# Kernel tuning notes

Hardware: AMD Instinct MI355X
Metric: run time of the kernel (lower is better)

## Reference

```python
import jax, jax.numpy as jnp
import numpy as np

C = 64
B, H, W = 2, 96, 96
EPS = 1e-5  # BatchNorm2d default eps


def conv1x1(x, w, b):
    # x: [B,C,H,W], w: [O,C], b: [O] -> [B,O,H,W]
    return jnp.einsum('bchw,oc->bohw', x, w) + b[None, :, None, None]


def setup_inputs() -> dict:
    key = jax.random.key(0)
    ks = jax.random.split(key, 12)
    s = 1.0 / np.sqrt(C)
    return {
        'x': jax.random.normal(ks[0], (B, C, H, W), dtype=jnp.float32),
        'g_w': jax.random.normal(ks[1], (C, C), dtype=jnp.float32) * s,
        'g_b': jax.random.normal(ks[2], (C,), dtype=jnp.float32) * s,
        'theta_w': jax.random.normal(ks[3], (C, C), dtype=jnp.float32) * s,
        'theta_b': jax.random.normal(ks[4], (C,), dtype=jnp.float32) * s,
        'phi_w': jax.random.normal(ks[5], (C, C), dtype=jnp.float32) * s,
        'phi_b': jax.random.normal(ks[6], (C,), dtype=jnp.float32) * s,
        'w_w': jax.random.normal(ks[7], (C, C), dtype=jnp.float32) * s,
        'w_b': jax.random.normal(ks[8], (C,), dtype=jnp.float32) * s,
        'bn_gamma': jnp.ones((C,), dtype=jnp.float32),
        'bn_beta': jnp.zeros((C,), dtype=jnp.float32),
        'bn_mean': jax.random.normal(ks[9], (C,), dtype=jnp.float32) * 0.1,
        'bn_var': jax.random.uniform(ks[10], (C,), dtype=jnp.float32, minval=0.5, maxval=1.5),
    }


def reference(x, g_w, g_b, theta_w, theta_b, phi_w, phi_b, w_w, w_b,
              bn_gamma, bn_beta, bn_mean, bn_var):
    b, c, h, w = x.shape
    n = h * w
    # 1x1 conv Q/K/V projections, flattened over spatial
    g_x = conv1x1(x, g_w, g_b).reshape(b, c, n).transpose(0, 2, 1)        # [B,N,C]
    theta_x = conv1x1(x, theta_w, theta_b).reshape(b, c, n).transpose(0, 2, 1)  # [B,N,C]
    phi_x = conv1x1(x, phi_w, phi_b).reshape(b, c, n)                      # [B,C,N]
    # full NxN attention: f = theta @ phi, softmax over last dim, y = f @ g
    f = jnp.einsum('bnc,bcm->bnm', theta_x, phi_x)                         # [B,N,N]
    attn = jax.nn.softmax(f, axis=-1)
    y = jnp.einsum('bnm,bmc->bnc', attn, g_x)                              # [B,N,C]
    y = y.transpose(0, 2, 1).reshape(b, c, h, w)
    # W: 1x1 conv + BatchNorm2d (inference: running stats) + residual
    w_y = conv1x1(y, w_w, w_b)
    inv_std = jax.lax.rsqrt(bn_var + EPS)
    w_y = (w_y - bn_mean[None, :, None, None]) * (bn_gamma * inv_std)[None, :, None, None] \
          + bn_beta[None, :, None, None]
    return w_y + x
```

## Files before the change

### kernel.cpp

```cpp
#include <hip/hip_runtime.h>
#include <hip/hip_bf16.h>

#define CC 64
#define NN 9216
#define NB 2
#define NQT 288
#define NKT 144

typedef __attribute__((ext_vector_type(4))) float f32x4;
typedef __attribute__((ext_vector_type(8))) short bf16x8;
typedef __attribute__((ext_vector_type(4))) unsigned int u32x4;

static __device__ __forceinline__ short f2bf(float f) {
    union { float f; unsigned u; } a; a.f = f;
    unsigned r = a.u + 0x7FFFu + ((a.u >> 16) & 1u);
    return (short)(r >> 16);
}

__global__ __launch_bounds__(256) void proj_kernel(
    const float* __restrict__ x,
    const float* __restrict__ gw, const float* __restrict__ gb,
    const float* __restrict__ tw, const float* __restrict__ tb,
    const float* __restrict__ pw, const float* __restrict__ pb,
    short* __restrict__ Qw, short* __restrict__ Kw, short* __restrict__ Vw)
{
    __shared__ float xs[64][68];
    const int b  = blockIdx.x / (NN / 64);
    const int n0 = (blockIdx.x % (NN / 64)) * 64;
    const int t  = threadIdx.x;

    {
        const int c = t >> 2, q = t & 3;
        const float* src = x + ((size_t)b * CC + c) * NN + n0 + q * 16;
        #pragma unroll
        for (int i = 0; i < 4; ++i) {
            float4 v = ((const float4*)src)[i];
            xs[c][q * 16 + i * 4 + 0] = v.x;
            xs[c][q * 16 + i * 4 + 1] = v.y;
            xs[c][q * 16 + i * 4 + 2] = v.z;
            xs[c][q * 16 + i * 4 + 3] = v.w;
        }
    }
    __syncthreads();

    const int n  = t & 63;
    const int og = __builtin_amdgcn_readfirstlane(t >> 6);
    float xr[64];
    #pragma unroll
    for (int c = 0; c < 64; ++c) xr[c] = xs[c][n];

    bf16x8 qv0, qv1, kv0, kv1;
    #pragma unroll
    for (int oi = 0; oi < 16; ++oi) {
        const int o = og * 16 + oi;
        float a0 = gb[o], a1 = tb[o], a2 = pb[o];
        #pragma unroll
        for (int c = 0; c < 64; ++c) {
            const float xv = xr[c];
            a0 += gw[o * 64 + c] * xv;
            a1 += tw[o * 64 + c] * xv;
            a2 += pw[o * 64 + c] * xv;
        }
        Vw[((size_t)b * CC + o) * NN + n0 + n] = f2bf(a0);
        if (oi < 8) { qv0[oi] = f2bf(a1); kv0[oi] = f2bf(a2); }
        else        { qv1[oi - 8] = f2bf(a1); kv1[oi - 8] = f2bf(a2); }
    }
    const size_t qkbase = ((size_t)b * NN + n0 + n) * CC + og * 16;
    *(bf16x8*)&Qw[qkbase]     = qv0;
    *(bf16x8*)&Qw[qkbase + 8] = qv1;
    *(bf16x8*)&Kw[qkbase]     = kv0;
    *(bf16x8*)&Kw[qkbase + 8] = kv1;
}

template<int SP>
__global__ __launch_bounds__(256) void attn_kernel(
    const short* __restrict__ Qw, const short* __restrict__ Kw,
    const short* __restrict__ Vw, float* __restrict__ Yp,
    float* __restrict__ Mp, float* __restrict__ Sp)
{
    constexpr int KCH = NKT / SP;
    const int gw  = blockIdx.x * 4 + (threadIdx.x >> 6);
    const int l   = threadIdx.x & 63;
    const int lr  = l & 15, lg = l >> 4;
    const int qt  = gw % NQT;
    const int rem = gw / NQT;
    const int b   = rem & 1;
    const int s   = rem >> 1;
    const int q0  = qt * 32;

    const short* Qb = Qw + (size_t)b * NN * CC;
    const short* Kb = Kw + (size_t)b * NN * CC;
    const short* Vb = Vw + (size_t)b * CC * NN;

    bf16x8 qf[2][2];
    #pragma unroll
    for (int qg = 0; qg < 2; ++qg)
        #pragma unroll
        for (int ch = 0; ch < 2; ++ch)
            qf[qg][ch] = *(const bf16x8*)(Qb + (size_t)(q0 + qg * 16 + lr) * CC + ch * 32 + lg * 8);

    f32x4 yacc[2][4];
    #pragma unroll
    for (int qg = 0; qg < 2; ++qg)
        #pragma unroll
        for (int u = 0; u < 4; ++u) yacc[qg][u] = (f32x4){0.f, 0.f, 0.f, 0.f};
    float m[2]  = {-1e30f, -1e30f};
    float se[2] = {0.f, 0.f};

    for (int kt = s * KCH; kt < s * KCH + KCH; ++kt) {
        const int jb = kt * 64;
        bf16x8 kf[4][2], vf[4][2];
        #pragma unroll
        for (int tt = 0; tt < 4; ++tt)
            #pragma unroll
            for (int ch = 0; ch < 2; ++ch)
                kf[tt][ch] = *(const bf16x8*)(Kb + (size_t)(jb + tt * 16 + lr) * CC + ch * 32 + lg * 8);
        #pragma unroll
        for (int u = 0; u < 4; ++u)
            #pragma unroll
            for (int jg = 0; jg < 2; ++jg)
                vf[u][jg] = *(const bf16x8*)(Vb + (size_t)(u * 16 + lr) * NN + jb + jg * 32 + lg * 8);

        #pragma unroll
        for (int qg = 0; qg < 2; ++qg) {
            f32x4 sv[4];
            #pragma unroll
            for (int tt = 0; tt < 4; ++tt) {
                f32x4 a = (f32x4){0.f, 0.f, 0.f, 0.f};
                a = __builtin_amdgcn_mfma_f32_16x16x32_bf16(kf[tt][0], qf[qg][0], a, 0, 0, 0);
                a = __builtin_amdgcn_mfma_f32_16x16x32_bf16(kf[tt][1], qf[qg][1], a, 0, 0, 0);
                sv[tt] = a;
            }
            float mx = -1e30f;
            #pragma unroll
            for (int tt = 0; tt < 4; ++tt)
                #pragma unroll
                for (int r = 0; r < 4; ++r) mx = fmaxf(mx, sv[tt][r]);
            mx = fmaxf(mx, __shfl_xor(mx, 16));
            mx = fmaxf(mx, __shfl_xor(mx, 32));
            const float mnew = fmaxf(m[qg], mx);
            const float scal = __expf(m[qg] - mnew);
            float rs = 0.f;
            unsigned p2[4][2];
            #pragma unroll
            for (int tt = 0; tt < 4; ++tt) {
                const float pa = __expf(sv[tt][0] - mnew);
                const float pb2 = __expf(sv[tt][1] - mnew);
                const float pc = __expf(sv[tt][2] - mnew);
                const float pd = __expf(sv[tt][3] - mnew);
                rs += (pa + pb2) + (pc + pd);
                p2[tt][0] = (unsigned)(unsigned short)f2bf(pa) | ((unsigned)(unsigned short)f2bf(pb2) << 16);
                p2[tt][1] = (unsigned)(unsigned short)f2bf(pc) | ((unsigned)(unsigned short)f2bf(pd) << 16);
            }
            rs += __shfl_xor(rs, 16);
            rs += __shfl_xor(rs, 32);
            se[qg] = se[qg] * scal + rs;
            m[qg]  = mnew;
            #pragma unroll
            for (int u = 0; u < 4; ++u) yacc[qg][u] *= scal;

            #pragma unroll
            for (int jg = 0; jg < 2; ++jg) {
                unsigned bfr[4];
                #pragma unroll
                for (int q = 0; q < 4; ++q) {
                    const int qh = q >> 1, h = q & 1;
                    const int src = lr | ((((lg << 1) + qh) & 3) << 4);
                    const int c0 = __shfl((int)p2[jg * 2 + 0][h], src);
                    const int c1 = __shfl((int)p2[jg * 2 + 1][h], src);
                    bfr[q] = (unsigned)((lg & 2) ? c1 : c0);
                }
                u32x4 bt = {bfr[0], bfr[1], bfr[2], bfr[3]};
                const bf16x8 pbf = __builtin_bit_cast(bf16x8, bt);
                #pragma unroll
                for (int u = 0; u < 4; ++u)
                    yacc[qg][u] = __builtin_amdgcn_mfma_f32_16x16x32_bf16(vf[u][jg], pbf, yacc[qg][u], 0, 0, 0);
            }
        }
    }

    const size_t pbase = (size_t)(s * NB + b) * NN;
    #pragma unroll
    for (int qg = 0; qg < 2; ++qg) {
        const int n = q0 + qg * 16 + lr;
        float* yrow = Yp + (pbase + n) * CC;
        #pragma unroll
        for (int u = 0; u < 4; ++u)
            *(f32x4*)&yrow[u * 16 + lg * 4] = yacc[qg][u];
        if (lg == 0) { Mp[pbase + n] = m[qg]; Sp[pbase + n] = se[qg]; }
    }
}

template<int SP>
__global__ __launch_bounds__(256) void out_kernel(
    const float* __restrict__ Yp, const float* __restrict__ Mp,
    const float* __restrict__ Sp, const float* __restrict__ x,
    const float* __restrict__ ww, const float* __restrict__ wb,
    const float* __restrict__ gam, const float* __restrict__ bet,
    const float* __restrict__ mu, const float* __restrict__ var,
    float* __restrict__ out)
{
    __shared__ float ys[64][65];
    __shared__ float wgt[SP][64];
    __shared__ float scl[64], shf[64];
    const int b  = blockIdx.x / (NN / 64);
    const int n0 = (blockIdx.x % (NN / 64)) * 64;
    const int t  = threadIdx.x;

    if (t < 64) {
        float e[SP], ssv[SP];
        float M = -1e30f;
        #pragma unroll
        for (int s = 0; s < SP; ++s) {
            e[s]   = Mp[(size_t)(s * NB + b) * NN + n0 + t];
            ssv[s] = Sp[(size_t)(s * NB + b) * NN + n0 + t];
            M = fmaxf(M, e[s]);
        }
        float den = 0.f;
        #pragma unroll
        for (int s = 0; s < SP; ++s) { e[s] = __expf(e[s] - M); den += e[s] * ssv[s]; }
        const float inv = 1.f / den;
        #pragma unroll
        for (int s = 0; s < SP; ++s) wgt[s][t] = e[s] * inv;
    } else if (t < 128) {
        const int c = t - 64;
        const float sc = gam[c] * rsqrtf(var[c] + 1e-5f);
        scl[c] = sc;
        shf[c] = bet[c] + (wb[c] - mu[c]) * sc;
    }
    __syncthreads();

    {
        const int n = t >> 2, q = t & 3;
        float acc[16];
        #pragma unroll
        for (int i = 0; i < 16; ++i) acc[i] = 0.f;
        #pragma unroll
        for (int s = 0; s < SP; ++s) {
            const float w = wgt[s][n];
            const float* src = Yp + ((size_t)(s * NB + b) * NN + n0 + n) * CC + q * 16;
            #pragma unroll
            for (int i = 0; i < 4; ++i) {
                const float4 v = ((const float4*)src)[i];
                acc[i * 4 + 0] += w * v.x;
                acc[i * 4 + 1] += w * v.y;
                acc[i * 4 + 2] += w * v.z;
                acc[i * 4 + 3] += w * v.w;
            }
        }
        #pragma unroll
        for (int i = 0; i < 16; ++i) ys[n][q * 16 + i] = acc[i];
    }
    __syncthreads();

    const int n  = t & 63;
    const int og = __builtin_amdgcn_readfirstlane(t >> 6);
    float yr[64];
    #pragma unroll
    for (int c = 0; c < 64; ++c) yr[c] = ys[n][c];

    #pragma unroll
    for (int oi = 0; oi < 16; ++oi) {
        const int o = og * 16 + oi;
        float a0 = 0.f, a1 = 0.f;
        #pragma unroll
        for (int c = 0; c < 64; c += 2) {
            a0 += ww[o * 64 + c]     * yr[c];
            a1 += ww[o * 64 + c + 1] * yr[c + 1];
        }
        const size_t oidx = ((size_t)b * CC + o) * NN + n0 + n;
        out[oidx] = (a0 + a1) * scl[o] + shf[o] + x[oidx];
    }
}

extern "C" void kernel_launch(void* const* d_in, const int* in_sizes, int n_in,
                              void* d_out, int out_size, void* d_ws, size_t ws_size,
                              hipStream_t stream) {
    const float* x    = (const float*)d_in[0];
    const float* g_w  = (const float*)d_in[1];
    const float* g_b  = (const float*)d_in[2];
    const float* th_w = (const float*)d_in[3];
    const float* th_b = (const float*)d_in[4];
    const float* ph_w = (const float*)d_in[5];
    const float* ph_b = (const float*)d_in[6];
    const float* w_w  = (const float*)d_in[7];
    const float* w_b  = (const float*)d_in[8];
    const float* bn_g = (const float*)d_in[9];
    const float* bn_b = (const float*)d_in[10];
    const float* bn_m = (const float*)d_in[11];
    const float* bn_v = (const float*)d_in[12];
    float* out = (float*)d_out;

    char* wsp = (char*)d_ws;
    short* Qw = (short*)(wsp);
    short* Kw = (short*)(wsp + 2359296);
    short* Vw = (short*)(wsp + 4718592);
    const size_t ypOff = 7077888;
    const size_t perSplit = 4718592 + 2 * 73728;
    int SP = 1;
    if (ws_size >= ypOff + 4 * perSplit) SP = 4;
    else if (ws_size >= ypOff + 2 * perSplit) SP = 2;
    float* Yp = (float*)(wsp + ypOff);
    float* Mp = (float*)(wsp + ypOff + (size_t)SP * 4718592);
    float* Sp = (float*)(wsp + ypOff + (size_t)SP * 4718592 + (size_t)SP * 73728);

    proj_kernel<<<NB * (NN / 64), 256, 0, stream>>>(x, g_w, g_b, th_w, th_b,
                                                    ph_w, ph_b, Qw, Kw, Vw);
    if (SP == 4) {
        attn_kernel<4><<<4 * 144, 256, 0, stream>>>(Qw, Kw, Vw, Yp, Mp, Sp);
        out_kernel<4><<<NB * (NN / 64), 256, 0, stream>>>(Yp, Mp, Sp, x, w_w, w_b,
                                                          bn_g, bn_b, bn_m, bn_v, out);
    } else if (SP == 2) {
        attn_kernel<2><<<2 * 144, 256, 0, stream>>>(Qw, Kw, Vw, Yp, Mp, Sp);
        out_kernel<2><<<NB * (NN / 64), 256, 0, stream>>>(Yp, Mp, Sp, x, w_w, w_b,
                                                          bn_g, bn_b, bn_m, bn_v, out);
    } else {
        attn_kernel<1><<<1 * 144, 256, 0, stream>>>(Qw, Kw, Vw, Yp, Mp, Sp);
        out_kernel<1><<<NB * (NN / 64), 256, 0, stream>>>(Yp, Mp, Sp, x, w_w, w_b,
                                                          bn_g, bn_b, bn_m, bn_v, out);
    }
}
```

Measured before the change: 360.3 us.

## Rework attention softmax/PV path, stage weights in LDS, add 8-way key split

```diff
diff --git a/kernel.cpp b/kernel.cpp
--- a/kernel.cpp
+++ b/kernel.cpp
@@ -6,15 +6,42 @@
 #define NB 2
 #define NQT 288
 #define NKT 144
+#define L2E 1.4426950408889634f
 
 typedef __attribute__((ext_vector_type(4))) float f32x4;
 typedef __attribute__((ext_vector_type(8))) short bf16x8;
-typedef __attribute__((ext_vector_type(4))) unsigned int u32x4;
+typedef __attribute__((ext_vector_type(4))) short bf16x4;
 
 static __device__ __forceinline__ short f2bf(float f) {
     union { float f; unsigned u; } a; a.f = f;
     unsigned r = a.u + 0x7FFFu + ((a.u >> 16) & 1u);
     return (short)(r >> 16);
+}
+
+static __device__ __forceinline__ unsigned cvtpk(float lo, float hi) {
+    unsigned r;
+    asm("v_cvt_pk_bf16_f32 %0, %1, %2" : "=v"(r) : "v"(lo), "v"(hi));
+    return r;
+}
+
+static __device__ __forceinline__ f32x4 mfma16(bf16x4 a, bf16x4 b, f32x4 c) {
+#if __has_builtin(__builtin_amdgcn_mfma_f32_16x16x16bf16_1k)
+    return __builtin_amdgcn_mfma_f32_16x16x16bf16_1k(a, b, c, 0, 0, 0);
+#elif __has_builtin(__builtin_amdgcn_mfma_f32_16x16x16_bf16)
+    return __builtin_amdgcn_mfma_f32_16x16x16_bf16(a, b, c, 0, 0, 0);
+#else
+    asm volatile("s_nop 1\n\tv_mfma_f32_16x16x16_bf16 %0, %1, %2, %0\n\ts_nop 7"
+                 : "+v"(c) : "v"(a), "v"(b));
+    return c;
+#endif
+}
+
+static __device__ __forceinline__ float ex2(float x) {
+#if __has_builtin(__builtin_amdgcn_exp2f)
+    return __builtin_amdgcn_exp2f(x);
+#else
+    return exp2f(x);
+#endif
 }
 
 __global__ __launch_bounds__(256) void proj_kernel(
@@ -25,9 +52,19 @@
     short* __restrict__ Qw, short* __restrict__ Kw, short* __restrict__ Vw)
 {
     __shared__ float xs[64][68];
+    __shared__ float wsm[3][64][64];
+    __shared__ float bsm[3][64];
     const int b  = blockIdx.x / (NN / 64);
     const int n0 = (blockIdx.x % (NN / 64)) * 64;
     const int t  = threadIdx.x;
+
+    float* wf = &wsm[0][0][0];
+    for (int i = t; i < 4096; i += 256) {
+        wf[i]        = gw[i];
+        wf[4096 + i] = tw[i];
+        wf[8192 + i] = pw[i];
+    }
+    if (t < 64) { bsm[0][t] = gb[t]; bsm[1][t] = tb[t]; bsm[2][t] = pb[t]; }
 
     {
         const int c = t >> 2, q = t & 3;
@@ -44,22 +81,21 @@
     __syncthreads();
 
     const int n  = t & 63;
-    const int og = __builtin_amdgcn_readfirstlane(t >> 6);
+    const int og = t >> 6;
     float xr[64];
     #pragma unroll
     for (int c = 0; c < 64; ++c) xr[c] = xs[c][n];
 
     bf16x8 qv0, qv1, kv0, kv1;
-    #pragma unroll
     for (int oi = 0; oi < 16; ++oi) {
         const int o = og * 16 + oi;
-        float a0 = gb[o], a1 = tb[o], a2 = pb[o];
+        float a0 = bsm[0][o], a1 = bsm[1][o], a2 = bsm[2][o];
         #pragma unroll
         for (int c = 0; c < 64; ++c) {
             const float xv = xr[c];
-            a0 += gw[o * 64 + c] * xv;
-            a1 += tw[o * 64 + c] * xv;
-            a2 += pw[o * 64 + c] * xv;
+            a0 += wsm[0][o][c] * xv;
+            a1 += wsm[1][o][c] * xv;
+            a2 += wsm[2][o][c] * xv;
         }
         Vw[((size_t)b * CC + o) * NN + n0 + n] = f2bf(a0);
         if (oi < 8) { qv0[oi] = f2bf(a1); kv0[oi] = f2bf(a2); }
@@ -85,7 +121,7 @@
     const int qt  = gw % NQT;
     const int rem = gw / NQT;
     const int b   = rem & 1;
-    const int s   = rem >> 1;
+    const int sp  = rem >> 1;
     const int q0  = qt * 32;
 
     const short* Qb = Qw + (size_t)b * NN * CC;
@@ -105,21 +141,24 @@
         #pragma unroll
         for (int u = 0; u < 4; ++u) yacc[qg][u] = (f32x4){0.f, 0.f, 0.f, 0.f};
     float m[2]  = {-1e30f, -1e30f};
+    float ml[2] = {-1e30f * L2E, -1e30f * L2E};
     float se[2] = {0.f, 0.f};
 
-    for (int kt = s * KCH; kt < s * KCH + KCH; ++kt) {
+    #pragma unroll 1
+    for (int kt = sp * KCH; kt < sp * KCH + KCH; ++kt) {
         const int jb = kt * 64;
-        bf16x8 kf[4][2], vf[4][2];
+        bf16x8 kf[4][2];
+        bf16x4 vA[4][4];
         #pragma unroll
         for (int tt = 0; tt < 4; ++tt)
             #pragma unroll
             for (int ch = 0; ch < 2; ++ch)
-                kf[tt][ch] = *(const bf16x8*)(Kb + (size_t)(jb + tt * 16 + lr) * CC + ch * 32 + lg * 8);
+                kf[tt][ch] = *(const bf16x8*)(Kb + (jb + tt * 16 + lr) * CC + ch * 32 + lg * 8);
         #pragma unroll
         for (int u = 0; u < 4; ++u)
             #pragma unroll
-            for (int jg = 0; jg < 2; ++jg)
-                vf[u][jg] = *(const bf16x8*)(Vb + (size_t)(u * 16 + lr) * NN + jb + jg * 32 + lg * 8);
+            for (int tt = 0; tt < 4; ++tt)
+                vA[u][tt] = *(const bf16x4*)(Vb + (u * 16 + lr) * NN + jb + tt * 16 + lg * 4);
 
         #pragma unroll
         for (int qg = 0; qg < 2; ++qg) {
@@ -138,48 +177,46 @@
                 for (int r = 0; r < 4; ++r) mx = fmaxf(mx, sv[tt][r]);
             mx = fmaxf(mx, __shfl_xor(mx, 16));
             mx = fmaxf(mx, __shfl_xor(mx, 32));
-            const float mnew = fmaxf(m[qg], mx);
-            const float scal = __expf(m[qg] - mnew);
+
+            if (__any(mx > m[qg] + 8.f)) {
+                const float mnew  = fmaxf(m[qg], mx);
+                const float mlnew = mnew * L2E;
+                const float scal  = ex2(ml[qg] - mlnew);
+                m[qg]  = mnew;
+                ml[qg] = mlnew;
+                se[qg] *= scal;
+                #pragma unroll
+                for (int u = 0; u < 4; ++u) yacc[qg][u] *= scal;
+            }
+
+            const float nml = -ml[qg];
             float rs = 0.f;
-            unsigned p2[4][2];
+            bf16x4 pbf[4];
             #pragma unroll
             for (int tt = 0; tt < 4; ++tt) {
-                const float pa = __expf(sv[tt][0] - mnew);
-                const float pb2 = __expf(sv[tt][1] - mnew);
-                const float pc = __expf(sv[tt][2] - mnew);
-                const float pd = __expf(sv[tt][3] - mnew);
-                rs += (pa + pb2) + (pc + pd);
-                p2[tt][0] = (unsigned)(unsigned short)f2bf(pa) | ((unsigned)(unsigned short)f2bf(pb2) << 16);
-                p2[tt][1] = (unsigned)(unsigned short)f2bf(pc) | ((unsigned)(unsigned short)f2bf(pd) << 16);
+                const float p0 = ex2(__builtin_fmaf(sv[tt][0], L2E, nml));
+                const float p1 = ex2(__builtin_fmaf(sv[tt][1], L2E, nml));
+                const float p2 = ex2(__builtin_fmaf(sv[tt][2], L2E, nml));
+                const float p3 = ex2(__builtin_fmaf(sv[tt][3], L2E, nml));
+                rs += (p0 + p1) + (p2 + p3);
+                union { unsigned u[2]; bf16x4 v; } pk;
+                pk.u[0] = cvtpk(p0, p1);
+                pk.u[1] = cvtpk(p2, p3);
+                pbf[tt] = pk.v;
             }
             rs += __shfl_xor(rs, 16);
             rs += __shfl_xor(rs, 32);
-            se[qg] = se[qg] * scal + rs;
-            m[qg]  = mnew;
-            #pragma unroll
-            for (int u = 0; u < 4; ++u) yacc[qg][u] *= scal;
-
-            #pragma unroll
-            for (int jg = 0; jg < 2; ++jg) {
-                unsigned bfr[4];
-                #pragma unroll
-                for (int q = 0; q < 4; ++q) {
-                    const int qh = q >> 1, h = q & 1;
-                    const int src = lr | ((((lg << 1) + qh) & 3) << 4);
-                    const int c0 = __shfl((int)p2[jg * 2 + 0][h], src);
-                    const int c1 = __shfl((int)p2[jg * 2 + 1][h], src);
-                    bfr[q] = (unsigned)((lg & 2) ? c1 : c0);
-                }
-                u32x4 bt = {bfr[0], bfr[1], bfr[2], bfr[3]};
-                const bf16x8 pbf = __builtin_bit_cast(bf16x8, bt);
+            se[qg] += rs;
+
+            #pragma unroll
+            for (int tt = 0; tt < 4; ++tt)
                 #pragma unroll
                 for (int u = 0; u < 4; ++u)
-                    yacc[qg][u] = __builtin_amdgcn_mfma_f32_16x16x32_bf16(vf[u][jg], pbf, yacc[qg][u], 0, 0, 0);
-            }
-        }
-    }
-
-    const size_t pbase = (size_t)(s * NB + b) * NN;
+                    yacc[qg][u] = mfma16(vA[u][tt], pbf[tt], yacc[qg][u]);
+        }
+    }
+
+    const size_t pbase = (size_t)(sp * NB + b) * NN;
     #pragma unroll
     for (int qg = 0; qg < 2; ++qg) {
         const int n = q0 + qg * 16 + lr;
@@ -201,12 +238,15 @@
     float* __restrict__ out)
 {
     __shared__ float ys[64][65];
+    __shared__ float wsm[64][64];
     __shared__ float wgt[SP][64];
     __shared__ float scl[64], shf[64];
     const int b  = blockIdx.x / (NN / 64);
     const int n0 = (blockIdx.x % (NN / 64)) * 64;
     const int t  = threadIdx.x;
 
+    float* wf = &wsm[0][0];
+    for (int i = t; i < 4096; i += 256) wf[i] = ww[i];
     if (t < 64) {
         float e[SP], ssv[SP];
         float M = -1e30f;
@@ -254,19 +294,18 @@
     __syncthreads();
 
     const int n  = t & 63;
-    const int og = __builtin_amdgcn_readfirstlane(t >> 6);
+    const int og = t >> 6;
     float yr[64];
     #pragma unroll
     for (int c = 0; c < 64; ++c) yr[c] = ys[n][c];
 
-    #pragma unroll
     for (int oi = 0; oi < 16; ++oi) {
         const int o = og * 16 + oi;
         float a0 = 0.f, a1 = 0.f;
         #pragma unroll
         for (int c = 0; c < 64; c += 2) {
-            a0 += ww[o * 64 + c]     * yr[c];
-            a1 += ww[o * 64 + c + 1] * yr[c + 1];
+            a0 += wsm[o][c]     * yr[c];
+            a1 += wsm[o][c + 1] * yr[c + 1];
         }
         const size_t oidx = ((size_t)b * CC + o) * NN + n0 + n;
         out[oidx] = (a0 + a1) * scl[o] + shf[o] + x[oidx];
@@ -298,7 +337,8 @@
     const size_t ypOff = 7077888;
     const size_t perSplit = 4718592 + 2 * 73728;
     int SP = 1;
-    if (ws_size >= ypOff + 4 * perSplit) SP = 4;
+    if      (ws_size >= ypOff + 8 * perSplit) SP = 8;
+    else if (ws_size >= ypOff + 4 * perSplit) SP = 4;
     else if (ws_size >= ypOff + 2 * perSplit) SP = 2;
     float* Yp = (float*)(wsp + ypOff);
     float* Mp = (float*)(wsp + ypOff + (size_t)SP * 4718592);
@@ -306,7 +346,11 @@
 
     proj_kernel<<<NB * (NN / 64), 256, 0, stream>>>(x, g_w, g_b, th_w, th_b,
                                                     ph_w, ph_b, Qw, Kw, Vw);
-    if (SP == 4) {
+    if (SP == 8) {
+        attn_kernel<8><<<8 * 144, 256, 0, stream>>>(Qw, Kw, Vw, Yp, Mp, Sp);
+        out_kernel<8><<<NB * (NN / 64), 256, 0, stream>>>(Yp, Mp, Sp, x, w_w, w_b,
+                                                          bn_g, bn_b, bn_m, bn_v, out);
+    } else if (SP == 4) {
         attn_kernel<4><<<4 * 144, 256, 0, stream>>>(Qw, Kw, Vw, Yp, Mp, Sp);
         out_kernel<4><<<NB * (NN / 64), 256, 0, stream>>>(Yp, Mp, Sp, x, w_w, w_b,
                                                           bn_g, bn_b, bn_m, bn_v, out);
```

Result: no change. 362.2 us (+0.5%).
